# Performance work log

Hardware: AMD Instinct MI355X
Metric: run time of the kernel (lower is better)

The kernel has to match this reference:

```python
import jax, jax.numpy as jnp
import numpy as np

B, T, D = 4, 2048, 2048
H = 16
DH = D // H  # 128
THETA = 10000.0


def _rope(x, offset=0):
    # x: [b, h, t, d]; lucidrains rotary_embedding_torch style (interleaved pairs)
    d = x.shape[-1]
    t = x.shape[-2]
    inv_freq = 1.0 / (THETA ** (jnp.arange(0, d, 2, dtype=jnp.float32) / d))  # [d/2]
    pos = jnp.arange(offset, offset + t, dtype=jnp.float32)
    freqs = pos[:, None] * inv_freq[None, :]              # [t, d/2]
    freqs = jnp.repeat(freqs, 2, axis=-1)                 # [t, d] (n r) interleave
    cos = jnp.cos(freqs).astype(x.dtype)
    sin = jnp.sin(freqs).astype(x.dtype)
    x1 = x[..., 0::2]
    x2 = x[..., 1::2]
    rot = jnp.stack([-x2, x1], axis=-1).reshape(x.shape)  # rotate_half
    return x * cos + rot * sin


def setup_inputs() -> dict:
    key = jax.random.key(0)
    ks = jax.random.split(key, 5)
    s = 1.0 / np.sqrt(D)
    return {
        "x": jax.random.normal(ks[0], (B, T, D), jnp.float32),
        "Wq": jax.random.normal(ks[1], (D, D), jnp.float32) * s,
        "Wk": jax.random.normal(ks[2], (D, D), jnp.float32) * s,
        "Wv": jax.random.normal(ks[3], (D, D), jnp.float32) * s,
        "Wo": jax.random.normal(ks[4], (D, D), jnp.float32) * s,
    }


def reference(x, Wq, Wk, Wv, Wo):
    b, t, d = x.shape
    # QKV projections (bias-free), split heads: b t (h f) -> b h t f
    q = (x @ Wq).reshape(b, t, H, DH).transpose(0, 2, 1, 3)
    k = (x @ Wk).reshape(b, t, H, DH).transpose(0, 2, 1, 3)
    v = (x @ Wv).reshape(b, t, H, DH).transpose(0, 2, 1, 3)
    # rotary embedding on q and k (offset = 0)
    q = _rope(q)
    k = _rope(k)
    # causal scaled dot-product attention
    scale = 1.0 / np.sqrt(DH)
    logits = jnp.einsum('bhtf,bhsf->bhts', q, k) * scale
    causal = jnp.tril(jnp.ones((t, t), dtype=bool))
    logits = jnp.where(causal, logits, jnp.finfo(logits.dtype).min)
    p = jax.nn.softmax(logits, axis=-1)
    y = jnp.einsum('bhts,bhsf->bhtf', p, v)
    # b h t f -> b t (h f), then output projection
    y = y.transpose(0, 2, 1, 3).reshape(b, t, d)
    return y @ Wo
```

## Files before the change

### kernel.cpp

```cpp
#include <hip/hip_runtime.h>
#include <hip/hip_bf16.h>
#include <math.h>

typedef unsigned short u16;
typedef __attribute__((ext_vector_type(8))) __bf16 bf16x8;
typedef __attribute__((ext_vector_type(4))) float f32x4;
typedef __attribute__((ext_vector_type(16))) float f32x16;
typedef __attribute__((ext_vector_type(8))) u16 u16x8;
typedef __attribute__((ext_vector_type(4))) u16 u16x4;
typedef __attribute__((ext_vector_type(4))) unsigned u32x4;

#define T_SEQ 2048
#define DMODEL 2048
#define NH 16
#define DHEAD 128
#define BATCH 4
#define ATTN_SCALE 0.08838834764831845f
#define QSCALE_LOG2E 0.1275411278534803f

#define GLOAD(gp, lp) __builtin_amdgcn_global_load_lds( \
    (const __attribute__((address_space(1))) void*)(gp), \
    (__attribute__((address_space(3))) void*)(lp), 16, 0, 0)

#define BAR() __builtin_amdgcn_s_barrier()
#define LGKM0() do { asm volatile("s_waitcnt lgkmcnt(0)" ::: "memory"); \
                     __builtin_amdgcn_sched_barrier(0); } while (0)
#define VMCNT4() asm volatile("s_waitcnt vmcnt(4)" ::: "memory")
#define MFMA32(A, B, C) __builtin_amdgcn_mfma_f32_32x32x16_bf16(A, B, C, 0, 0, 0)

__device__ __forceinline__ float b2f(u16 u) {
  union { float f; unsigned int i; } x; x.i = ((unsigned int)u) << 16; return x.f;
}
__device__ __forceinline__ u16 f2b(float f) {
  __bf16 h = (__bf16)f;
  return *(u16*)&h;
}
__device__ __forceinline__ unsigned pk2(float lo, float hi2) {
  __bf16 a = (__bf16)lo, b = (__bf16)hi2;
  unsigned short ua = *(unsigned short*)&a, ub = *(unsigned short*)&b;
  return (unsigned)ua | ((unsigned)ub << 16);
}

__global__ __launch_bounds__(256) void cast_f32_bf16(const float* __restrict__ in,
                                                     u16* __restrict__ out) {
  long i = ((long)blockIdx.x * 256 + threadIdx.x) * 8;
  float4 a = *(const float4*)(in + i);
  float4 b = *(const float4*)(in + i + 4);
  u16x8 r;
  r[0] = f2b(a.x); r[1] = f2b(a.y); r[2] = f2b(a.z); r[3] = f2b(a.w);
  r[4] = f2b(b.x); r[5] = f2b(b.y); r[6] = f2b(b.z); r[7] = f2b(b.w);
  *(u16x8*)(out + i) = r;
}

__global__ __launch_bounds__(256) void wtrans_kernel(const float* __restrict__ W,
                                                     u16* __restrict__ Wt) {
  __shared__ float tile[64][65];
  const int k0 = blockIdx.x * 64, n0 = blockIdx.y * 64;
  const int c = threadIdx.x & 63, r4 = threadIdx.x >> 6;
#pragma unroll
  for (int p = 0; p < 16; p++) {
    int r = p * 4 + r4;
    tile[r][c] = W[(long)(k0 + r) * DMODEL + n0 + c];
  }
  __syncthreads();
#pragma unroll
  for (int p = 0; p < 16; p++) {
    int r = p * 4 + r4;
    Wt[(long)(n0 + r) * DMODEL + k0 + c] = f2b(tile[c][r]);
  }
}

__global__ __launch_bounds__(256) void vtrans_kernel(const u16* __restrict__ V,
                                                     u16* __restrict__ Vt) {
  __shared__ u16 tile[64][66];
  const int s0 = blockIdx.x * 64, f0 = blockIdx.y * 64;
  const int bh = blockIdx.z;
  const int b = bh >> 4, h = bh & 15;
  const int c = threadIdx.x & 63, r4 = threadIdx.x >> 6;
#pragma unroll
  for (int p = 0; p < 16; p++) {
    int r = p * 4 + r4;
    tile[r][c] = V[(long)(b * T_SEQ + s0 + r) * DMODEL + h * DHEAD + f0 + c];
  }
  __syncthreads();
#pragma unroll
  for (int p = 0; p < 16; p++) {
    int r = p * 4 + r4;
    Vt[(long)(bh * DHEAD + f0 + r) * T_SEQ + s0 + c] = tile[c][r];
  }
}

__global__ __launch_bounds__(256) void rope_kernel(u16* __restrict__ X) {
  int idx = blockIdx.x * 256 + threadIdx.x;
  int i4 = idx & 15;
  int h = (idx >> 4) & 15;
  long bt = idx >> 8;
  int t = (int)(bt & (T_SEQ - 1));
  long off = bt * DMODEL + h * DHEAD + i4 * 8;
  u16x8 v = *(u16x8*)(X + off);
  float o[8];
#pragma unroll
  for (int j = 0; j < 4; j++) {
    int i = i4 * 4 + j;
    float inv = __builtin_amdgcn_exp2f((float)i * -0.20762050593045857f);
    float ang = (float)t * inv;
    float cs = cosf(ang), sn = sinf(ang);
    float x0 = b2f(v[2 * j]), x1 = b2f(v[2 * j + 1]);
    o[2 * j]     = x0 * cs - x1 * sn;
    o[2 * j + 1] = x1 * cs + x0 * sn;
  }
  u16x8 r;
#pragma unroll
  for (int j = 0; j < 8; j++) r[j] = f2b(o[j]);
  *(u16x8*)(X + off) = r;
}

#define LOAD_A(q)                                                      \
  _Pragma("unroll") for (int k = 0; k < 2; k++)                        \
  _Pragma("unroll") for (int m = 0; m < 2; m++) {                      \
    int r = wr * 128 + (q) * 32 + m * 16 + lr;                         \
    int cc = (k * 4 + lc) ^ (r & 7);                                   \
    a[k][m] = *(const bf16x8*)&sA[par][r * 64 + cc * 8];               \
  }

#define LOAD_B()                                                       \
  _Pragma("unroll") for (int k = 0; k < 2; k++)                        \
  _Pragma("unroll") for (int n = 0; n < 4; n++) {                      \
    int r = wc * 64 + n * 16 + lr;                                     \
    int cc = (k * 4 + lc) ^ (r & 7);                                   \
    b[k][n] = *(const bf16x8*)&sB[par][r * 64 + cc * 8];               \
  }

#define MFMA_QUAD(q)                                                   \
  _Pragma("unroll") for (int k = 0; k < 2; k++)                        \
  _Pragma("unroll") for (int n = 0; n < 4; n++)                        \
  _Pragma("unroll") for (int m = 0; m < 2; m++)                        \
    acc[(q) * 2 + m][n] = __builtin_amdgcn_mfma_f32_16x16x32_bf16(     \
        a[k][m], b[k][n], acc[(q) * 2 + m][n], 0, 0, 0);

#define STAGE_HALF(g, ldsp, rc0, t_, h_)                               \
  _Pragma("unroll") for (int j = 0; j < 2; j++) {                      \
    int rl = (h_) * 128 + wid * 16 + j * 8 + (lane >> 3);              \
    int cc = (lane & 7) ^ (lane >> 3);                                 \
    GLOAD((g) + ((rc0) + rl) * (long)K + (long)(t_) * 64 + cc * 8,     \
          (ldsp) + (h_) * 128 * 64 + (wid * 16 + j * 8) * 64);         \
  }

template <int OUT_F32>
__global__ __launch_bounds__(512, 2) void gemm_bt(const u16* __restrict__ A,
                                                  const u16* __restrict__ Bt,
                                                  void* __restrict__ Cv,
                                                  int M, int N, int K) {
  __shared__ u16 sA[2][256 * 64];
  __shared__ u16 sB[2][256 * 64];
  const int tid = threadIdx.x, lane = tid & 63, wid = tid >> 6;
  const int wr = wid >> 2, wc = wid & 3;
  const int lr = lane & 15, lc = lane >> 4;
  const int id = blockIdx.x;
  const long row0 = (long)(id >> 3) * 256;
  const long col0 = (long)(id & 7) * 256;
  const int NT = K >> 6;

  f32x4 acc[8][4] = {};
  bf16x8 a[2][2], b[2][4];

  STAGE_HALF(Bt, &sB[0][0], col0, 0, 0);
  STAGE_HALF(Bt, &sB[0][0], col0, 0, 1);
  STAGE_HALF(A,  &sA[0][0], row0, 0, 0);
  STAGE_HALF(A,  &sA[0][0], row0, 0, 1);
  STAGE_HALF(Bt, &sB[1][0], col0, 1, 0);
  STAGE_HALF(Bt, &sB[1][0], col0, 1, 1);
  VMCNT4();
  BAR();

  for (int t = 0; t < NT; t++) {
    const int par = t & 1;
    LOAD_B();
    LOAD_A(0);
    if (t + 1 < NT) { STAGE_HALF(A, &sA[par ^ 1][0], row0, t + 1, 0); }
    BAR(); LGKM0();
    __builtin_amdgcn_s_setprio(1); MFMA_QUAD(0); __builtin_amdgcn_s_setprio(0);
    BAR();
    LOAD_A(1);
    if (t + 1 < NT) { STAGE_HALF(A, &sA[par ^ 1][0], row0, t + 1, 1); }
    if (t + 2 < NT) { STAGE_HALF(Bt, &sB[par][0], col0, t + 2, 0); }
    BAR(); LGKM0();
    __builtin_amdgcn_s_setprio(1); MFMA_QUAD(1); __builtin_amdgcn_s_setprio(0);
    BAR();
    LOAD_A(2);
    if (t + 2 < NT) { STAGE_HALF(Bt, &sB[par][0], col0, t + 2, 1); }
    BAR(); LGKM0();
    __builtin_amdgcn_s_setprio(1); MFMA_QUAD(2); __builtin_amdgcn_s_setprio(0);
    BAR();
    LOAD_A(3);
    VMCNT4();
    BAR(); LGKM0();
    __builtin_amdgcn_s_setprio(1); MFMA_QUAD(3); __builtin_amdgcn_s_setprio(0);
    BAR();
  }

#pragma unroll
  for (int mf = 0; mf < 8; mf++)
#pragma unroll
    for (int n = 0; n < 4; n++)
#pragma unroll
      for (int i = 0; i < 4; i++) {
        long row = row0 + wr * 128 + mf * 16 + lc * 4 + i;
        long col = col0 + wc * 64 + n * 16 + lr;
        float v = acc[mf][n][i];
        if (OUT_F32) ((float*)Cv)[row * N + col] = v;
        else ((u16*)Cv)[row * N + col] = f2b(v);
      }
}

__global__ __launch_bounds__(256, 2) void attn_kernel(const u16* __restrict__ Q,
                                                      const u16* __restrict__ K,
                                                      const u16* __restrict__ Vt,
                                                      u16* __restrict__ Y) {
  __shared__ u16 lK[2][64 * 128];
  __shared__ u16 lV[2][128 * 64];
  const int tid = threadIdx.x, lane = tid & 63, w = tid >> 6;
  const int hi = lane >> 5, l31 = lane & 31;
  const int id = blockIdx.x;
  const int qt = 15 - (id >> 6);
  const int bh = id & 63;
  const int b = bh >> 4, h = bh & 15;
  const int qg = qt * 128 + w * 32 + l31;
  const int swz = l31 & 7;

  bf16x8 qf[8];
  const long qrow = (long)(b * T_SEQ + qg) * DMODEL + h * DHEAD;
#pragma unroll
  for (int kd = 0; kd < 8; kd++) {
    u16x8 raw = *(const u16x8*)(Q + qrow + kd * 16 + hi * 8);
    bf16x8 q;
#pragma unroll
    for (int j = 0; j < 8; j++) q[j] = (__bf16)(b2f(raw[j]) * QSCALE_LOG2E);
    qf[kd] = q;
  }

  f32x16 o0 = {}, o1 = {}, o2 = {}, o3 = {};
  float m_st = -INFINITY, l_st = 0.f;
  const int nt = (qt + 1) * 2;

#define STAGE(nb, kt_)                                                              \
  {                                                                                 \
    _Pragma("unroll")                                                               \
    for (int j = 0; j < 4; j++) {                                                   \
      int sb = (w * 4 + j) * 64;                                                    \
      int slot = sb + lane;                                                         \
      { int r = slot >> 4, pc = slot & 15, cc = pc ^ (r & 7);                       \
        GLOAD(K + (long)(b * T_SEQ + (kt_) * 64 + r) * DMODEL + h * DHEAD + cc * 8, \
              &lK[nb][sb * 8]); }                                                   \
      { int r = slot >> 3, pc = slot & 7, cc = pc ^ (r & 7);                        \
        GLOAD(Vt + (long)(bh * DHEAD + r) * T_SEQ + (kt_) * 64 + cc * 8,            \
              &lV[nb][sb * 8]); }                                                   \
    }                                                                               \
  }

  STAGE(0, 0);
  __syncthreads();

  for (int kt = 0; kt < nt; kt++) {
    const int cur = kt & 1;
    if (kt + 1 < nt) STAGE(cur ^ 1, kt + 1);

    f32x16 st0 = {}, st1 = {};
    __builtin_amdgcn_s_setprio(1);
#pragma unroll
    for (int kd = 0; kd < 8; kd++) {
      int pc = (kd * 2 + hi) ^ swz;
      bf16x8 kf0 = *(const bf16x8*)&lK[cur][l31 * 128 + pc * 8];
      bf16x8 kf1 = *(const bf16x8*)&lK[cur][(32 + l31) * 128 + pc * 8];
      st0 = MFMA32(kf0, qf[kd], st0);
      st1 = MFMA32(kf1, qf[kd], st1);
    }
    __builtin_amdgcn_s_setprio(0);

    if (kt * 64 + 63 > qt * 128 + w * 32) {
#pragma unroll
      for (int r = 0; r < 16; r++) {
        int sl = kt * 64 + (r & 3) + 8 * (r >> 2) + 4 * hi;
        if (sl > qg) st0[r] = -1e30f;
        if (sl + 32 > qg) st1[r] = -1e30f;
      }
    }

    float mx = -1e30f;
#pragma unroll
    for (int r = 0; r < 16; r++) mx = fmaxf(mx, fmaxf(st0[r], st1[r]));
    mx = fmaxf(mx, __shfl_xor(mx, 32, 64));
    if (__any(mx > m_st + 8.0f)) {
      float mnew = fmaxf(m_st, mx);
      float corr = __builtin_amdgcn_exp2f(m_st - mnew);
      m_st = mnew;
      l_st *= corr;
#pragma unroll
      for (int r = 0; r < 16; r++) {
        o0[r] *= corr; o1[r] *= corr; o2[r] *= corr; o3[r] *= corr;
      }
    }
    float rs = 0.f;
#pragma unroll
    for (int r = 0; r < 16; r++) {
      st0[r] = __builtin_amdgcn_exp2f(st0[r] - m_st); rs += st0[r];
      st1[r] = __builtin_amdgcn_exp2f(st1[r] - m_st); rs += st1[r];
    }
    rs += __shfl_xor(rs, 32, 64);
    l_st += rs;

    __builtin_amdgcn_s_setprio(1);
#define PVHALF(stX, sb)                                                        \
    _Pragma("unroll")                                                          \
    for (int g = 0; g < 2; g++) {                                              \
      unsigned A0 = pk2(stX[8 * g + 0], stX[8 * g + 1]);                       \
      unsigned A1 = pk2(stX[8 * g + 2], stX[8 * g + 3]);                       \
      unsigned B0 = pk2(stX[8 * g + 4], stX[8 * g + 5]);                       \
      unsigned B1 = pk2(stX[8 * g + 6], stX[8 * g + 7]);                       \
      unsigned xA0 = __shfl_xor(A0, 32, 64);                                   \
      unsigned xA1 = __shfl_xor(A1, 32, 64);                                   \
      unsigned xB0 = __shfl_xor(B0, 32, 64);                                   \
      unsigned xB1 = __shfl_xor(B1, 32, 64);                                   \
      u32x4 pw;                                                                \
      pw[0] = hi ? xB0 : A0;                                                   \
      pw[1] = hi ? xB1 : A1;                                                   \
      pw[2] = hi ? B0 : xA0;                                                   \
      pw[3] = hi ? B1 : xA1;                                                   \
      bf16x8 pa = *(bf16x8*)&pw;                                               \
      const int ks = (sb) * 2 + g;                                             \
      int pc0 = (ks * 2 + hi) ^ swz;                                           \
      bf16x8 vb0 = *(const bf16x8*)&lV[cur][(l31) * 64 + pc0 * 8];             \
      o0 = MFMA32(vb0, pa, o0);                                                \
      bf16x8 vb1 = *(const bf16x8*)&lV[cur][(32 + l31) * 64 + pc0 * 8];        \
      o1 = MFMA32(vb1, pa, o1);                                                \
      bf16x8 vb2 = *(const bf16x8*)&lV[cur][(64 + l31) * 64 + pc0 * 8];        \
      o2 = MFMA32(vb2, pa, o2);                                                \
      bf16x8 vb3 = *(const bf16x8*)&lV[cur][(96 + l31) * 64 + pc0 * 8];        \
      o3 = MFMA32(vb3, pa, o3);                                                \
    }
    PVHALF(st0, 0)
    PVHALF(st1, 1)
#undef PVHALF
    __builtin_amdgcn_s_setprio(0);

    __syncthreads();
  }

  float inv = __builtin_amdgcn_rcpf(l_st);
#define WR(oN, n)                                                              \
  _Pragma("unroll")                                                            \
  for (int rq = 0; rq < 4; rq++) {                                             \
    u16x4 pk;                                                                  \
    _Pragma("unroll")                                                          \
    for (int j = 0; j < 4; j++) pk[j] = f2b(oN[rq * 4 + j] * inv);             \
    *(u16x4*)(Y + qrow + (n) * 32 + rq * 8 + hi * 4) = pk;                     \
  }
  WR(o0, 0) WR(o1, 1) WR(o2, 2) WR(o3, 3)
#undef WR
#undef STAGE
}

extern "C" void kernel_launch(void* const* d_in, const int* in_sizes, int n_in,
                              void* d_out, int out_size, void* d_ws, size_t ws_size,
                              hipStream_t stream) {
  const float* x  = (const float*)d_in[0];
  const float* Wq = (const float*)d_in[1];
  const float* Wk = (const float*)d_in[2];
  const float* Wv = (const float*)d_in[3];
  const float* Wo = (const float*)d_in[4];
  float* out = (float*)d_out;
  char* ws = (char*)d_ws;

  const long MB32 = 33554432L;
  u16* xb  = (u16*)(ws);
  u16* Wqt = (u16*)(ws + MB32);
  u16* Wkt = (u16*)(ws + MB32 + 8388608L);
  u16* Wvt = (u16*)(ws + MB32 + 16777216L);
  u16* Wot = (u16*)(ws + MB32 + 25165824L);
  u16* Qb  = (u16*)(ws + 2 * MB32);
  u16* Kb  = (u16*)(ws + 3 * MB32);
  u16* Vb  = (u16*)(ws + 4 * MB32);
  u16* Vtb = xb;
  u16* Yb  = Vb;

  cast_f32_bf16<<<8192, 256, 0, stream>>>(x, xb);
  dim3 wt_g(32, 32);
  wtrans_kernel<<<wt_g, 256, 0, stream>>>(Wq, Wqt);
  wtrans_kernel<<<wt_g, 256, 0, stream>>>(Wk, Wkt);
  wtrans_kernel<<<wt_g, 256, 0, stream>>>(Wv, Wvt);
  wtrans_kernel<<<wt_g, 256, 0, stream>>>(Wo, Wot);

  gemm_bt<0><<<256, 512, 0, stream>>>(xb, Wqt, Qb, 8192, 2048, 2048);
  gemm_bt<0><<<256, 512, 0, stream>>>(xb, Wkt, Kb, 8192, 2048, 2048);
  gemm_bt<0><<<256, 512, 0, stream>>>(xb, Wvt, Vb, 8192, 2048, 2048);

  rope_kernel<<<8192, 256, 0, stream>>>(Qb);
  rope_kernel<<<8192, 256, 0, stream>>>(Kb);

  dim3 vt_g(32, 2, 64);
  vtrans_kernel<<<vt_g, 256, 0, stream>>>(Vb, Vtb);

  attn_kernel<<<1024, 256, 0, stream>>>(Qb, Kb, Vtb, Yb);

  gemm_bt<1><<<256, 512, 0, stream>>>(Yb, Wot, (void*)out, 8192, 2048, 2048);
}
```

Measured before the change: 470.1 us.

## Fuse Q/K/V projections into one GEMM with interleaved QKV output buffer

```diff
diff --git a/kernel.cpp b/kernel.cpp
--- a/kernel.cpp
+++ b/kernel.cpp
@@ -15,6 +15,7 @@
 #define NH 16
 #define DHEAD 128
 #define BATCH 4
+#define QKV_STR 6144
 #define ATTN_SCALE 0.08838834764831845f
 #define QSCALE_LOG2E 0.1275411278534803f
 
@@ -70,7 +71,7 @@
   }
 }
 
-__global__ __launch_bounds__(256) void vtrans_kernel(const u16* __restrict__ V,
+__global__ __launch_bounds__(256) void vtrans_kernel(const u16* __restrict__ C,
                                                      u16* __restrict__ Vt) {
   __shared__ u16 tile[64][66];
   const int s0 = blockIdx.x * 64, f0 = blockIdx.y * 64;
@@ -80,7 +81,7 @@
 #pragma unroll
   for (int p = 0; p < 16; p++) {
     int r = p * 4 + r4;
-    tile[r][c] = V[(long)(b * T_SEQ + s0 + r) * DMODEL + h * DHEAD + f0 + c];
+    tile[r][c] = C[(long)(b * T_SEQ + s0 + r) * QKV_STR + 4096 + h * DHEAD + f0 + c];
   }
   __syncthreads();
 #pragma unroll
@@ -90,13 +91,13 @@
   }
 }
 
-__global__ __launch_bounds__(256) void rope_kernel(u16* __restrict__ X) {
+__global__ __launch_bounds__(256) void rope_qk_kernel(u16* __restrict__ X) {
   int idx = blockIdx.x * 256 + threadIdx.x;
-  int i4 = idx & 15;
-  int h = (idx >> 4) & 15;
-  long bt = idx >> 8;
-  int t = (int)(bt & (T_SEQ - 1));
-  long off = bt * DMODEL + h * DHEAD + i4 * 8;
+  int c8 = idx & 511;
+  long row = idx >> 9;
+  int t = (int)(row & (T_SEQ - 1));
+  int i4 = c8 & 15;
+  long off = row * QKV_STR + (long)c8 * 8;
   u16x8 v = *(u16x8*)(X + off);
   float o[8];
 #pragma unroll
@@ -138,16 +139,16 @@
     acc[(q) * 2 + m][n] = __builtin_amdgcn_mfma_f32_16x16x32_bf16(     \
         a[k][m], b[k][n], acc[(q) * 2 + m][n], 0, 0, 0);
 
-#define STAGE_HALF(g, ldsp, rc0, t_, h_)                               \
+#define STAGE_HALF(g, ld, ldsp, rc0, t_, h_)                           \
   _Pragma("unroll") for (int j = 0; j < 2; j++) {                      \
     int rl = (h_) * 128 + wid * 16 + j * 8 + (lane >> 3);              \
     int cc = (lane & 7) ^ (lane >> 3);                                 \
-    GLOAD((g) + ((rc0) + rl) * (long)K + (long)(t_) * 64 + cc * 8,     \
+    GLOAD((g) + ((rc0) + rl) * (long)(ld) + (long)(t_) * 64 + cc * 8,  \
           (ldsp) + (h_) * 128 * 64 + (wid * 16 + j * 8) * 64);         \
   }
 
 template <int OUT_F32>
-__global__ __launch_bounds__(512, 2) void gemm_bt(const u16* __restrict__ A,
+__global__ __launch_bounds__(512, 2) void gemm_bt(const u16* __restrict__ A, long lda,
                                                   const u16* __restrict__ Bt,
                                                   void* __restrict__ Cv,
                                                   int M, int N, int K) {
@@ -157,19 +158,21 @@
   const int wr = wid >> 2, wc = wid & 3;
   const int lr = lane & 15, lc = lane >> 4;
   const int id = blockIdx.x;
-  const long row0 = (long)(id >> 3) * 256;
-  const long col0 = (long)(id & 7) * 256;
+  const int per = (N >> 8) >> 3;
+  const int g8 = id >> 3;
+  const long col0 = (long)((id & 7) + 8 * (g8 % per)) * 256;
+  const long row0 = (long)(g8 / per) * 256;
   const int NT = K >> 6;
 
   f32x4 acc[8][4] = {};
   bf16x8 a[2][2], b[2][4];
 
-  STAGE_HALF(Bt, &sB[0][0], col0, 0, 0);
-  STAGE_HALF(Bt, &sB[0][0], col0, 0, 1);
-  STAGE_HALF(A,  &sA[0][0], row0, 0, 0);
-  STAGE_HALF(A,  &sA[0][0], row0, 0, 1);
-  STAGE_HALF(Bt, &sB[1][0], col0, 1, 0);
-  STAGE_HALF(Bt, &sB[1][0], col0, 1, 1);
+  STAGE_HALF(Bt, K, &sB[0][0], col0, 0, 0);
+  STAGE_HALF(Bt, K, &sB[0][0], col0, 0, 1);
+  STAGE_HALF(A, lda, &sA[0][0], row0, 0, 0);
+  STAGE_HALF(A, lda, &sA[0][0], row0, 0, 1);
+  STAGE_HALF(Bt, K, &sB[1][0], col0, 1, 0);
+  STAGE_HALF(Bt, K, &sB[1][0], col0, 1, 1);
   VMCNT4();
   BAR();
 
@@ -177,18 +180,18 @@
     const int par = t & 1;
     LOAD_B();
     LOAD_A(0);
-    if (t + 1 < NT) { STAGE_HALF(A, &sA[par ^ 1][0], row0, t + 1, 0); }
+    if (t + 1 < NT) { STAGE_HALF(A, lda, &sA[par ^ 1][0], row0, t + 1, 0); }
     BAR(); LGKM0();
     __builtin_amdgcn_s_setprio(1); MFMA_QUAD(0); __builtin_amdgcn_s_setprio(0);
     BAR();
     LOAD_A(1);
-    if (t + 1 < NT) { STAGE_HALF(A, &sA[par ^ 1][0], row0, t + 1, 1); }
-    if (t + 2 < NT) { STAGE_HALF(Bt, &sB[par][0], col0, t + 2, 0); }
+    if (t + 1 < NT) { STAGE_HALF(A, lda, &sA[par ^ 1][0], row0, t + 1, 1); }
+    if (t + 2 < NT) { STAGE_HALF(Bt, K, &sB[par][0], col0, t + 2, 0); }
     BAR(); LGKM0();
     __builtin_amdgcn_s_setprio(1); MFMA_QUAD(1); __builtin_amdgcn_s_setprio(0);
     BAR();
     LOAD_A(2);
-    if (t + 2 < NT) { STAGE_HALF(Bt, &sB[par][0], col0, t + 2, 1); }
+    if (t + 2 < NT) { STAGE_HALF(Bt, K, &sB[par][0], col0, t + 2, 1); }
     BAR(); LGKM0();
     __builtin_amdgcn_s_setprio(1); MFMA_QUAD(2); __builtin_amdgcn_s_setprio(0);
     BAR();
@@ -213,10 +216,8 @@
       }
 }
 
-__global__ __launch_bounds__(256, 2) void attn_kernel(const u16* __restrict__ Q,
-                                                      const u16* __restrict__ K,
-                                                      const u16* __restrict__ Vt,
-                                                      u16* __restrict__ Y) {
+__global__ __launch_bounds__(256, 2) void attn_kernel(const u16* __restrict__ QK,
+                                                      const u16* __restrict__ Vt) {
   __shared__ u16 lK[2][64 * 128];
   __shared__ u16 lV[2][128 * 64];
   const int tid = threadIdx.x, lane = tid & 63, w = tid >> 6;
@@ -229,10 +230,10 @@
   const int swz = l31 & 7;
 
   bf16x8 qf[8];
-  const long qrow = (long)(b * T_SEQ + qg) * DMODEL + h * DHEAD;
+  const long qrow = (long)(b * T_SEQ + qg) * QKV_STR + h * DHEAD;
 #pragma unroll
   for (int kd = 0; kd < 8; kd++) {
-    u16x8 raw = *(const u16x8*)(Q + qrow + kd * 16 + hi * 8);
+    u16x8 raw = *(const u16x8*)(QK + qrow + kd * 16 + hi * 8);
     bf16x8 q;
 #pragma unroll
     for (int j = 0; j < 8; j++) q[j] = (__bf16)(b2f(raw[j]) * QSCALE_LOG2E);
@@ -250,7 +251,8 @@
       int sb = (w * 4 + j) * 64;                                                    \
       int slot = sb + lane;                                                         \
       { int r = slot >> 4, pc = slot & 15, cc = pc ^ (r & 7);                       \
-        GLOAD(K + (long)(b * T_SEQ + (kt_) * 64 + r) * DMODEL + h * DHEAD + cc * 8, \
+        GLOAD(QK + (long)(b * T_SEQ + (kt_) * 64 + r) * QKV_STR + 2048 +            \
+                  h * DHEAD + cc * 8,                                               \
               &lK[nb][sb * 8]); }                                                   \
       { int r = slot >> 3, pc = slot & 7, cc = pc ^ (r & 7);                        \
         GLOAD(Vt + (long)(bh * DHEAD + r) * T_SEQ + (kt_) * 64 + cc * 8,            \
@@ -306,8 +308,7 @@
       st0[r] = __builtin_amdgcn_exp2f(st0[r] - m_st); rs += st0[r];
       st1[r] = __builtin_amdgcn_exp2f(st1[r] - m_st); rs += st1[r];
     }
-    rs += __shfl_xor(rs, 32, 64);
-    l_st += rs;
+    l_st += rs + __shfl_xor(rs, 32, 64);
 
     __builtin_amdgcn_s_setprio(1);
 #define PVHALF(stX, sb)                                                        \
@@ -353,7 +354,7 @@
     u16x4 pk;                                                                  \
     _Pragma("unroll")                                                          \
     for (int j = 0; j < 4; j++) pk[j] = f2b(oN[rq * 4 + j] * inv);             \
-    *(u16x4*)(Y + qrow + (n) * 32 + rq * 8 + hi * 4) = pk;                     \
+    *(u16x4*)((u16*)QK + qrow + 4096 + (n) * 32 + rq * 8 + hi * 4) = pk;       \
   }
   WR(o0, 0) WR(o1, 1) WR(o2, 2) WR(o3, 3)
 #undef WR
@@ -371,17 +372,14 @@
   float* out = (float*)d_out;
   char* ws = (char*)d_ws;
 
-  const long MB32 = 33554432L;
-  u16* xb  = (u16*)(ws);
-  u16* Wqt = (u16*)(ws + MB32);
-  u16* Wkt = (u16*)(ws + MB32 + 8388608L);
-  u16* Wvt = (u16*)(ws + MB32 + 16777216L);
-  u16* Wot = (u16*)(ws + MB32 + 25165824L);
-  u16* Qb  = (u16*)(ws + 2 * MB32);
-  u16* Kb  = (u16*)(ws + 3 * MB32);
-  u16* Vb  = (u16*)(ws + 4 * MB32);
-  u16* Vtb = xb;
-  u16* Yb  = Vb;
+  const long MB = 1048576L;
+  u16* xb   = (u16*)(ws);
+  u16* Wqt  = (u16*)(ws + 32 * MB);
+  u16* Wkt  = (u16*)(ws + 40 * MB);
+  u16* Wvt  = (u16*)(ws + 48 * MB);
+  u16* Wot  = (u16*)(ws + 56 * MB);
+  u16* Cqkv = (u16*)(ws + 64 * MB);
+  u16* Vtb  = xb;
 
   cast_f32_bf16<<<8192, 256, 0, stream>>>(x, xb);
   dim3 wt_g(32, 32);
@@ -390,17 +388,15 @@
   wtrans_kernel<<<wt_g, 256, 0, stream>>>(Wv, Wvt);
   wtrans_kernel<<<wt_g, 256, 0, stream>>>(Wo, Wot);
 
-  gemm_bt<0><<<256, 512, 0, stream>>>(xb, Wqt, Qb, 8192, 2048, 2048);
-  gemm_bt<0><<<256, 512, 0, stream>>>(xb, Wkt, Kb, 8192, 2048, 2048);
-  gemm_bt<0><<<256, 512, 0, stream>>>(xb, Wvt, Vb, 8192, 2048, 2048);
-
-  rope_kernel<<<8192, 256, 0, stream>>>(Qb);
-  rope_kernel<<<8192, 256, 0, stream>>>(Kb);
+  gemm_bt<0><<<768, 512, 0, stream>>>(xb, 2048, Wqt, Cqkv, 8192, 6144, 2048);
+
+  rope_qk_kernel<<<16384, 256, 0, stream>>>(Cqkv);
 
   dim3 vt_g(32, 2, 64);
-  vtrans_kernel<<<vt_g, 256, 0, stream>>>(Vb, Vtb);
-
-  attn_kernel<<<1024, 256, 0, stream>>>(Qb, Kb, Vtb, Yb);
-
-  gemm_bt<1><<<256, 512, 0, stream>>>(Yb, Wot, (void*)out, 8192, 2048, 2048);
-}
+  vtrans_kernel<<<vt_g, 256, 0, stream>>>(Cqkv, Vtb);
+
+  attn_kernel<<<1024, 256, 0, stream>>>(Cqkv, Vtb);
+
+  gemm_bt<1><<<256, 512, 0, stream>>>(Cqkv + 4096, QKV_STR, Wot, (void*)out,
+                                      8192, 2048, 2048);
+}
```

New measurement: 451.8 us. -3.9%, faster.
